# Optimization experiments

Measured on AMD Instinct MI355X. Metric: run time of the kernel, lower is better.

Reference implementation:

```python
import jax, jax.numpy as jnp
import numpy as np

N, E, IN_C, HID, HEADS, OUT_C, NG = 50000, 800000, 300, 64, 2, 2, 256


def _lin(key, fan_in, fan_out):
    k1, k2 = jax.random.split(key)
    lim = 1.0 / np.sqrt(fan_in)
    W = jax.random.uniform(k1, (fan_in, fan_out), jnp.float32, -lim, lim)
    b = jax.random.uniform(k2, (fan_out,), jnp.float32, -lim, lim)
    return W, b


def setup_inputs() -> dict:
    key = jax.random.key(0)
    ks = jax.random.split(key, 16)
    x = jax.random.normal(ks[0], (N, IN_C), jnp.float32)
    edge_index = jax.random.randint(ks[1], (2, E), 0, N, jnp.int64)
    batch = jnp.sort(jax.random.randint(ks[2], (N,), 0, NG, jnp.int64))
    d = {"x": x, "edge_index": edge_index, "batch": batch}
    d["syn_W"], d["syn_b"] = _lin(ks[3], IN_C, HID)
    d["ant_W"], d["ant_b"] = _lin(ks[4], IN_C, HID)
    d["fus_W"], d["fus_b"] = _lin(ks[5], 2 * HID, HID * HEADS)
    # conv1: in=HID*HEADS, out=HID, heads=HEADS (concat)
    d["c1_Wq"], d["c1_bq"] = _lin(ks[6], HID * HEADS, HEADS * HID)
    d["c1_Wk"], d["c1_bk"] = _lin(ks[7], HID * HEADS, HEADS * HID)
    d["c1_Wv"], d["c1_bv"] = _lin(ks[8], HID * HEADS, HEADS * HID)
    d["c1_Ws"], d["c1_bs"] = _lin(ks[9], HID * HEADS, HEADS * HID)
    # conv2: in=HID*HEADS, out=HID, heads=1
    d["c2_Wq"], d["c2_bq"] = _lin(ks[10], HID * HEADS, HID)
    d["c2_Wk"], d["c2_bk"] = _lin(ks[11], HID * HEADS, HID)
    d["c2_Wv"], d["c2_bv"] = _lin(ks[12], HID * HEADS, HID)
    d["c2_Ws"], d["c2_bs"] = _lin(ks[13], HID * HEADS, HID)
    d["l1_W"], d["l1_b"] = _lin(ks[14], HID, HID)
    d["l2_W"], d["l2_b"] = _lin(ks[15], HID, OUT_C)
    return d


def transformer_conv(x, src, dst, Wq, bq, Wk, bk, Wv, bv, Ws, bs, heads, d_head):
    # PyG TransformerConv (concat=True, root_weight=True, eval mode)
    q = (x @ Wq + bq).reshape(-1, heads, d_head)  # [N,H,D]
    k = (x @ Wk + bk).reshape(-1, heads, d_head)
    v = (x @ Wv + bv).reshape(-1, heads, d_head)
    qi = q[dst]  # [E,H,D]
    kj = k[src]
    vj = v[src]
    alpha = jnp.einsum("ehd,ehd->eh", qi, kj) / jnp.sqrt(jnp.float32(d_head))
    amax = jax.ops.segment_max(alpha, dst, num_segments=x.shape[0])
    ealpha = jnp.exp(alpha - amax[dst])
    denom = jax.ops.segment_sum(ealpha, dst, num_segments=x.shape[0])
    alpha = ealpha / (denom[dst] + 1e-16)
    out = jax.ops.segment_sum(alpha[..., None] * vj, dst, num_segments=x.shape[0])
    out = out.reshape(x.shape[0], heads * d_head)
    return out + x @ Ws + bs


def reference(x, edge_index, batch, syn_W, syn_b, ant_W, ant_b, fus_W, fus_b,
              c1_Wq, c1_bq, c1_Wk, c1_bk, c1_Wv, c1_bv, c1_Ws, c1_bs,
              c2_Wq, c2_bq, c2_Wk, c2_bk, c2_Wv, c2_bv, c2_Ws, c2_bs,
              l1_W, l1_b, l2_W, l2_b):
    src, dst = edge_index[0], edge_index[1]
    x_syn = jax.nn.relu(x @ syn_W + syn_b)
    x_ant = jax.nn.relu(x @ ant_W + ant_b)
    x_fused = jnp.concatenate([x_syn, x_ant], axis=1) @ fus_W + fus_b  # [N, HID*HEADS]
    h = transformer_conv(x_fused, src, dst, c1_Wq, c1_bq, c1_Wk, c1_bk,
                         c1_Wv, c1_bv, c1_Ws, c1_bs, HEADS, HID)
    h = jax.nn.relu(h)
    h = transformer_conv(h, src, dst, c2_Wq, c2_bq, c2_Wk, c2_bk,
                         c2_Wv, c2_bv, c2_Ws, c2_bs, 1, HID)
    # global mean pool over graphs
    sums = jax.ops.segment_sum(h, batch, num_segments=NG)
    cnts = jax.ops.segment_sum(jnp.ones((h.shape[0], 1), h.dtype), batch, num_segments=NG)
    pooled = sums / jnp.maximum(cnts, 1.0)
    out = jax.nn.relu(pooled @ l1_W + l1_b)
    return out @ l2_W + l2_b
```

## Files before the change

kernel.cpp:

```cpp
#include <hip/hip_runtime.h>
#include <math.h>

#define NNODES 50000
#define NEDGES 800000
#define INC    300
#define NGRAPH 256

typedef __attribute__((ext_vector_type(8))) short bf16x8;
typedef __attribute__((ext_vector_type(4))) short bf16x4;
typedef __attribute__((ext_vector_type(4))) float f32x4;

#define L2E8 0.180336880f
#define SW(row, k) ((k) ^ (((row) & 7) << 3))
#define EB 3125
#define FRONT_BLOCKS 782
#define FF_GRID (FRONT_BLOCKS + EB)

__device__ __forceinline__ unsigned short f2bf(float f) {
    unsigned u = __float_as_uint(f);
    u += 0x7fffu + ((u >> 16) & 1u);
    return (unsigned short)(u >> 16);
}
__device__ __forceinline__ float bf2f(unsigned short h) {
    return __uint_as_float(((unsigned)h) << 16);
}

struct WTArgs {
    const float* w[11];
    unsigned short* o[11];
    int K[11];
    int N[11];
    int mode[11];
    int roff[11];
    const float* syn_b; const float* ant_b;
    const float* c1q; const float* c1k; const float* c1v; const float* c1s;
    const float* c2q; const float* c2k; const float* c2v; const float* c2s;
    float* enc_b;
    float* c1_b;
    float* c2_b;
};

__global__ void k_setup(WTArgs a, const int* __restrict__ dstv, int* __restrict__ deg) {
    int bx = blockIdx.x;
    if (bx < EB) {
        int e = bx * 256 + threadIdx.x;
        if (e < NEDGES) atomicAdd(&deg[dstv[e]], 1);
        return;
    }
    bx -= EB;
    int which = bx / 75;
    int sub = bx - which * 75;
    if (which == 11) {
        if (sub != 0) return;
        int t = threadIdx.x;
        for (int u = t; u < 896; u += 256) {
            if (u < 512) {
                int s = u >> 7, r = u & 127;
                const float* p = (s == 0) ? a.c1q : (s == 1) ? a.c1k : (s == 2) ? a.c1v : a.c1s;
                a.c1_b[u] = p[r];
            } else if (u < 768) {
                int v = u - 512;
                int s = v >> 6, r = v & 63;
                const float* p = (s == 0) ? a.c2q : (s == 1) ? a.c2k : (s == 2) ? a.c2v : a.c2s;
                a.c2_b[v] = p[r];
            } else {
                int v = u - 768;
                a.enc_b[v] = (v < 64) ? a.syn_b[v] : a.ant_b[v - 64];
            }
        }
        return;
    }
    int i = sub * 256 + threadIdx.x;
    int K = a.K[which], N = a.N[which];
    if (i >= K * N) return;
    int k = i / N, n = i - k * N;
    unsigned short v = f2bf(a.w[which][i]);
    size_t dst;
    int m = a.mode[which];
    if (m == 1) {
        int row = a.roff[which] + n;
        dst = (size_t)(k >> 6) * 8192 + row * 64 + SW(row, k & 63);
    } else if (m == 2) {
        dst = (size_t)n * 128 + SW(n, k);
    } else {
        dst = (size_t)n * K + k;
    }
    a.o[which][dst] = v;
}

__global__ void k_scan1(const int* __restrict__ deg, int* __restrict__ ex,
                        int* __restrict__ bsum, int n) {
    __shared__ int tmp[256];
    int i = blockIdx.x * 256 + threadIdx.x;
    int v = (i < n) ? deg[i] : 0;
    tmp[threadIdx.x] = v;
    __syncthreads();
    for (int off = 1; off < 256; off <<= 1) {
        int t = (threadIdx.x >= off) ? tmp[threadIdx.x - off] : 0;
        __syncthreads();
        tmp[threadIdx.x] += t;
        __syncthreads();
    }
    if (i < n) ex[i] = tmp[threadIdx.x] - v;
    if (threadIdx.x == 255) bsum[blockIdx.x] = tmp[255];
}

__global__ void k_scan2(int* __restrict__ bsum, int nb) {
    __shared__ int tmp[256];
    int v = (threadIdx.x < nb) ? bsum[threadIdx.x] : 0;
    tmp[threadIdx.x] = v;
    __syncthreads();
    for (int off = 1; off < 256; off <<= 1) {
        int t = (threadIdx.x >= off) ? tmp[threadIdx.x - off] : 0;
        __syncthreads();
        tmp[threadIdx.x] += t;
        __syncthreads();
    }
    if (threadIdx.x < nb) bsum[threadIdx.x] = tmp[threadIdx.x] - v;
}

__global__ void k_scan3(int* __restrict__ rp, const int* __restrict__ bsum,
                        int* __restrict__ cursor, int n, int E) {
    int i = blockIdx.x * 256 + threadIdx.x;
    if (i < n) {
        int r = rp[i] + bsum[blockIdx.x];
        rp[i] = r;
        cursor[i] = r;
    }
    if (i == 0) rp[n] = E;
}

__global__ __launch_bounds__(256) void k_front_fill(
    const float* __restrict__ x,
    const unsigned short* __restrict__ enc_img, const float* __restrict__ enc_b,
    const unsigned short* __restrict__ fus_img, const float* __restrict__ fus_b,
    const unsigned short* __restrict__ c1_img, const float* __restrict__ c1_b,
    unsigned short* __restrict__ qkvs1, int M,
    const int* __restrict__ src, const int* __restrict__ dstv,
    int* __restrict__ cursor, int* __restrict__ esrc)
{
    const int b = blockIdx.x;
    const int q = b / 5, r5 = b - q * 5;
    const int tid = threadIdx.x;
    if (!(r5 == 0 && q < FRONT_BLOCKS)) {
        int nf = (b + 4) / 5;
        if (nf > FRONT_BLOCKS) nf = FRONT_BLOCKS;
        int e = (b - nf) * 256 + tid;
        if (e < NEDGES) {
            int d = dstv[e];
            int p = atomicAdd(&cursor[d], 1);
            esrc[p] = src[e];
        }
        return;
    }
    __shared__ __align__(16) short P[24576];
    short* bufI = P;
    short* B0   = P + 8192;
    short* B1   = P + 16384;
    short* Bt   = P + 8192;
    const int bm = q * 64;
    const int l  = tid & 63;
    const int wv = tid >> 6;
    const int fr = l & 15;
    const int fg = l >> 4;

    bf16x8 aP[10];
    {
        int row = bm + wv * 16 + fr;
        if (row >= M) row = M - 1;
        const float* xr = x + (size_t)row * INC + fg * 8;
        #pragma unroll
        for (int t = 0; t < 9; ++t) {
            float4 u0 = *reinterpret_cast<const float4*>(xr + t * 32);
            float4 u1 = *reinterpret_cast<const float4*>(xr + t * 32 + 4);
            bf16x8 f;
            f[0] = (short)f2bf(u0.x); f[1] = (short)f2bf(u0.y);
            f[2] = (short)f2bf(u0.z); f[3] = (short)f2bf(u0.w);
            f[4] = (short)f2bf(u1.x); f[5] = (short)f2bf(u1.y);
            f[6] = (short)f2bf(u1.z); f[7] = (short)f2bf(u1.w);
            aP[t] = f;
        }
        bf16x8 f9 = (bf16x8){0, 0, 0, 0, 0, 0, 0, 0};
        int c0 = 288 + fg * 8;
        #pragma unroll
        for (int j = 0; j < 8; ++j) {
            int c = c0 + j;
            if (c < INC) f9[j] = (short)f2bf(x[(size_t)row * INC + c]);
        }
        aP[9] = f9;
    }

    f32x4 acc1[8];
    #pragma unroll
    for (int j = 0; j < 8; ++j) acc1[j] = (f32x4){0.f, 0.f, 0.f, 0.f};

    {
        bf16x8* d = (bf16x8*)B0;
        const bf16x8* s = (const bf16x8*)enc_img;
        #pragma unroll
        for (int i = 0; i < 4; ++i) d[tid + i * 256] = s[tid + i * 256];
    }
    __syncthreads();
    for (int ph = 0; ph < 5; ++ph) {
        short* cur = (ph & 1) ? B1 : B0;
        short* nxt = (ph & 1) ? B0 : B1;
        bf16x8 tmp[4];
        if (ph < 4) {
            const bf16x8* s = (const bf16x8*)(enc_img + (ph + 1) * 8192);
            #pragma unroll
            for (int i = 0; i < 4; ++i) tmp[i] = s[tid + i * 256];
        }
        #pragma unroll
        for (int ks = 0; ks < 2; ++ks) {
            int kk = ks * 32 + fg * 8;
            int t = ph * 2 + ks;
            #pragma unroll
            for (int nj = 0; nj < 8; ++nj) {
                int br = nj * 16 + fr;
                bf16x8 bfr = *reinterpret_cast<const bf16x8*>(cur + br * 64 + SW(br, kk));
                acc1[nj] = __builtin_amdgcn_mfma_f32_16x16x32_bf16(aP[t], bfr, acc1[nj], 0, 0, 0);
            }
        }
        if (ph < 4) {
            bf16x8* d = (bf16x8*)nxt;
            #pragma unroll
            for (int i = 0; i < 4; ++i) d[tid + i * 256] = tmp[i];
        }
        __syncthreads();
    }
    #pragma unroll
    for (int nj = 0; nj < 8; ++nj) {
        int col = nj * 16 + fr;
        float bv = enc_b[col];
        #pragma unroll
        for (int r = 0; r < 4; ++r) {
            int row = wv * 16 + fg * 4 + r;
            float val = fmaxf(acc1[nj][r] + bv, 0.f);
            bufI[row * 128 + SW(row, col)] = (short)f2bf(val);
        }
    }
    __syncthreads();

    bf16x8 af[4];
    {
        int ar = wv * 16 + fr;
        #pragma unroll
        for (int t = 0; t < 4; ++t)
            af[t] = *reinterpret_cast<const bf16x8*>(bufI + ar * 128 + SW(ar, fg * 8 + t * 32));
    }
    __syncthreads();
    {
        bf16x8* d = (bf16x8*)Bt;
        const bf16x8* s = (const bf16x8*)fus_img;
        #pragma unroll
        for (int i = 0; i < 8; ++i) d[tid + i * 256] = s[tid + i * 256];
    }
    __syncthreads();

    f32x4 acc2[8];
    #pragma unroll
    for (int j = 0; j < 8; ++j) acc2[j] = (f32x4){0.f, 0.f, 0.f, 0.f};
    #pragma unroll
    for (int t = 0; t < 4; ++t) {
        int k = t * 32 + fg * 8;
        #pragma unroll
        for (int nj = 0; nj < 8; ++nj) {
            int br = nj * 16 + fr;
            bf16x8 bfr = *reinterpret_cast<const bf16x8*>(Bt + br * 128 + SW(br, k));
            acc2[nj] = __builtin_amdgcn_mfma_f32_16x16x32_bf16(af[t], bfr, acc2[nj], 0, 0, 0);
        }
    }
    __syncthreads();
    #pragma unroll
    for (int nj = 0; nj < 8; ++nj) {
        int col = nj * 16 + fr;
        float bv = fus_b[col];
        #pragma unroll
        for (int r = 0; r < 4; ++r) {
            int row = wv * 16 + fg * 4 + r;
            bufI[row * 128 + SW(row, col)] = (short)f2bf(acc2[nj][r] + bv);
        }
    }
    __syncthreads();

    bf16x8 af2[4];
    {
        int ar = wv * 16 + fr;
        #pragma unroll
        for (int t = 0; t < 4; ++t)
            af2[t] = *reinterpret_cast<const bf16x8*>(bufI + ar * 128 + SW(ar, fg * 8 + t * 32));
    }

    #pragma unroll
    for (int cc = 0; cc < 4; ++cc) {
        __syncthreads();
        {
            bf16x8* d = (bf16x8*)Bt;
            const bf16x8* s = (const bf16x8*)(c1_img + cc * 16384);
            #pragma unroll
            for (int i = 0; i < 8; ++i) d[tid + i * 256] = s[tid + i * 256];
        }
        __syncthreads();
        f32x4 acc3[8];
        #pragma unroll
        for (int j = 0; j < 8; ++j) acc3[j] = (f32x4){0.f, 0.f, 0.f, 0.f};
        #pragma unroll
        for (int t = 0; t < 4; ++t) {
            int k = t * 32 + fg * 8;
            #pragma unroll
            for (int nj = 0; nj < 8; ++nj) {
                int br = nj * 16 + fr;
                bf16x8 bfr = *reinterpret_cast<const bf16x8*>(Bt + br * 128 + SW(br, k));
                acc3[nj] = __builtin_amdgcn_mfma_f32_16x16x32_bf16(af2[t], bfr, acc3[nj], 0, 0, 0);
            }
        }
        #pragma unroll
        for (int nj = 0; nj < 8; ++nj) {
            int col = nj * 16 + fr;
            float bv = c1_b[cc * 128 + col];
            #pragma unroll
            for (int r = 0; r < 4; ++r) {
                int row = wv * 16 + fg * 4 + r;
                bufI[row * 128 + col] = (short)f2bf(acc3[nj][r] + bv);
            }
        }
        __syncthreads();
        #pragma unroll
        for (int i = 0; i < 4; ++i) {
            int p = tid + i * 256;
            int row = p >> 4;
            int c8 = (p & 15) * 8;
            int gr = bm + row;
            if (gr < M)
                *reinterpret_cast<bf16x8*>(qkvs1 + (size_t)gr * 512 + cc * 128 + c8) =
                    *reinterpret_cast<const bf16x8*>(bufI + row * 128 + c8);
        }
    }
}

#define BM 128

template<int BNT>
__global__ __launch_bounds__(256) void gemm_mfma(
    const unsigned short* __restrict__ A, int lda, int M, int K,
    const unsigned short* __restrict__ Wt,
    const float* __restrict__ bias,
    unsigned short* __restrict__ C, int ldc)
{
    __shared__ __align__(16) short As[BM * 64];
    __shared__ __align__(16) short Bs[BNT * 64];
    const int tid = threadIdx.x;
    const int bm = blockIdx.x * BM;
    const int bn = blockIdx.y * BNT;
    const int tr = tid >> 4;
    const int tc = (tid & 15) * 4;
    const int l  = tid & 63;
    const int wv = tid >> 6;
    const int fr = l & 15;
    const int fg = l >> 4;

    f32x4 acc[2][BNT / 16];
    #pragma unroll
    for (int i = 0; i < 2; ++i)
        #pragma unroll
        for (int j = 0; j < BNT / 16; ++j) acc[i][j] = (f32x4){0.f, 0.f, 0.f, 0.f};

    for (int k0 = 0; k0 < K; k0 += 64) {
        #pragma unroll
        for (int p = 0; p < 8; ++p) {
            int row = p * 16 + tr;
            int grow = bm + row;
            int k = k0 + tc;
            bf16x4 s4 = (bf16x4){0, 0, 0, 0};
            if (grow < M) s4 = *reinterpret_cast<const bf16x4*>(A + (size_t)grow * lda + k);
            *reinterpret_cast<bf16x4*>(As + row * 64 + SW(row, tc)) = s4;
        }
        #pragma unroll
        for (int p = 0; p < BNT / 16; ++p) {
            int n = p * 16 + tr;
            *reinterpret_cast<bf16x4*>(Bs + n * 64 + SW(n, tc)) =
                *reinterpret_cast<const bf16x4*>(Wt + (size_t)(bn + n) * K + k0 + tc);
        }
        __syncthreads();
        #pragma unroll
        for (int ks = 0; ks < 2; ++ks) {
            int kk = ks * 32 + fg * 8;
            int ar0 = wv * 32 + fr, ar1 = wv * 32 + 16 + fr;
            bf16x8 a0 = *reinterpret_cast<const bf16x8*>(As + ar0 * 64 + SW(ar0, kk));
            bf16x8 a1 = *reinterpret_cast<const bf16x8*>(As + ar1 * 64 + SW(ar1, kk));
            #pragma unroll
            for (int nj = 0; nj < BNT / 16; ++nj) {
                int br = nj * 16 + fr;
                bf16x8 b = *reinterpret_cast<const bf16x8*>(Bs + br * 64 + SW(br, kk));
                acc[0][nj] = __builtin_amdgcn_mfma_f32_16x16x32_bf16(a0, b, acc[0][nj], 0, 0, 0);
                acc[1][nj] = __builtin_amdgcn_mfma_f32_16x16x32_bf16(a1, b, acc[1][nj], 0, 0, 0);
            }
        }
        __syncthreads();
    }
    #pragma unroll
    for (int mi = 0; mi < 2; ++mi) {
        #pragma unroll
        for (int nj = 0; nj < BNT / 16; ++nj) {
            int col = nj * 16 + fr;
            float bv = bias[bn + col];
            #pragma unroll
            for (int r = 0; r < 4; ++r) {
                int lr = wv * 16 + fg * 4 + r;
                As[lr * BNT + col] = (short)f2bf(acc[mi][nj][r] + bv);
            }
        }
        __syncthreads();
        #pragma unroll
        for (int i = 0; i < 4; ++i) {
            int p = tid + i * 256;
            int lr = p >> 4;
            int c8 = (p & 15) * 8;
            int grow = bm + (lr >> 4) * 32 + mi * 16 + (lr & 15);
            if (grow < M)
                *reinterpret_cast<bf16x8*>(C + (size_t)grow * ldc + bn + c8) =
                    *reinterpret_cast<const bf16x8*>(As + lr * BNT + c8);
        }
        __syncthreads();
    }
}

__global__ __launch_bounds__(256) void attn_h2(
    const unsigned short* __restrict__ qkvs,
    const int* __restrict__ rowptr, const int* __restrict__ esrc,
    unsigned short* __restrict__ outp, int N)
{
    int wid = (blockIdx.x * blockDim.x + threadIdx.x) >> 6;
    int l = threadIdx.x & 63;
    if (wid >= N) return;
    const int sl = l & 15;
    const int g  = l >> 4;
    const unsigned short* bi = qkvs + (size_t)wid * 512;
    float q[8];
    {
        bf16x8 qv = *reinterpret_cast<const bf16x8*>(bi + 8 * sl);
        #pragma unroll
        for (int i = 0; i < 8; ++i) q[i] = bf2f((unsigned short)qv[i]) * L2E8;
    }
    float s = 0.f;
    float acc[8] = {0.f, 0.f, 0.f, 0.f, 0.f, 0.f, 0.f, 0.f};
    const int beg = rowptr[wid], end = rowptr[wid + 1];
    const int iters = (end - beg + 3) >> 2;
    int e = beg + g;
    bool va0 = e < end;
    int j0 = va0 ? esrc[e] : wid;
    const unsigned short* pp0 = qkvs + (size_t)j0 * 512 + 8 * sl;
    bf16x8 ka = *reinterpret_cast<const bf16x8*>(pp0 + 128);
    bf16x8 vva = *reinterpret_cast<const bf16x8*>(pp0 + 256);
    bool va1 = (e + 4) < end;
    int j1 = va1 ? esrc[e + 4] : wid;
    const unsigned short* pp1 = qkvs + (size_t)j1 * 512 + 8 * sl;
    bf16x8 kb = *reinterpret_cast<const bf16x8*>(pp1 + 128);
    bf16x8 vvb = *reinterpret_cast<const bf16x8*>(pp1 + 256);
    for (int it = 0; it < iters; ++it) {
        bf16x8 kc = ka, vc = vva;
        bool vd = va0;
        ka = kb; vva = vvb; va0 = va1;
        va1 = (e + 8) < end;
        int j2 = va1 ? esrc[e + 8] : wid;
        const unsigned short* p2 = qkvs + (size_t)j2 * 512 + 8 * sl;
        kb = *reinterpret_cast<const bf16x8*>(p2 + 128);
        vvb = *reinterpret_cast<const bf16x8*>(p2 + 256);
        e += 4;
        float p = 0.f;
        #pragma unroll
        for (int i = 0; i < 8; ++i) p += q[i] * bf2f((unsigned short)kc[i]);
        p += __shfl_xor(p, 1, 64);
        p += __shfl_xor(p, 2, 64);
        p += __shfl_xor(p, 4, 64);
        float w = vd ? __builtin_amdgcn_exp2f(p) : 0.f;
        s += w;
        #pragma unroll
        for (int i = 0; i < 8; ++i) acc[i] += w * bf2f((unsigned short)vc[i]);
    }
    #pragma unroll
    for (int mask = 16; mask <= 32; mask <<= 1) {
        s += __shfl_xor(s, mask, 64);
        #pragma unroll
        for (int i = 0; i < 8; ++i) acc[i] += __shfl_xor(acc[i], mask, 64);
    }
    if (g == 0) {
        float inv = 1.f / (s + 1e-16f);
        bf16x8 sv = *reinterpret_cast<const bf16x8*>(bi + 384 + 8 * sl);
        bf16x8 o;
        #pragma unroll
        for (int i = 0; i < 8; ++i) {
            float r = fmaxf(acc[i] * inv + bf2f((unsigned short)sv[i]), 0.f);
            o[i] = (short)f2bf(r);
        }
        *reinterpret_cast<bf16x8*>(outp + (size_t)wid * 128 + 8 * sl) = o;
    }
}

__global__ __launch_bounds__(256) void attn_h1(
    const unsigned short* __restrict__ qkvs,
    const int* __restrict__ rowptr, const int* __restrict__ esrc,
    float* __restrict__ outp, int N)
{
    int wid = (blockIdx.x * blockDim.x + threadIdx.x) >> 6;
    int l = threadIdx.x & 63;
    if (wid >= N) return;
    const int sl = l & 7;
    const int g  = l >> 3;
    const unsigned short* bi = qkvs + (size_t)wid * 256;
    float q[8];
    {
        bf16x8 qv = *reinterpret_cast<const bf16x8*>(bi + 8 * sl);
        #pragma unroll
        for (int i = 0; i < 8; ++i) q[i] = bf2f((unsigned short)qv[i]) * L2E8;
    }
    float s = 0.f;
    float acc[8] = {0.f, 0.f, 0.f, 0.f, 0.f, 0.f, 0.f, 0.f};
    const int beg = rowptr[wid], end = rowptr[wid + 1];
    const int iters = (end - beg + 7) >> 3;
    int e = beg + g;
    bool va0 = e < end;
    int j0 = va0 ? esrc[e] : wid;
    const unsigned short* pp0 = qkvs + (size_t)j0 * 256 + 8 * sl;
    bf16x8 ka = *reinterpret_cast<const bf16x8*>(pp0 + 64);
    bf16x8 vva = *reinterpret_cast<const bf16x8*>(pp0 + 128);
    bool va1 = (e + 8) < end;
    int j1 = va1 ? esrc[e + 8] : wid;
    const unsigned short* pp1 = qkvs + (size_t)j1 * 256 + 8 * sl;
    bf16x8 kb = *reinterpret_cast<const bf16x8*>(pp1 + 64);
    bf16x8 vvb = *reinterpret_cast<const bf16x8*>(pp1 + 128);
    for (int it = 0; it < iters; ++it) {
        bf16x8 kc = ka, vc = vva;
        bool vd = va0;
        ka = kb; vva = vvb; va0 = va1;
        va1 = (e + 16) < end;
        int j2 = va1 ? esrc[e + 16] : wid;
        const unsigned short* p2 = qkvs + (size_t)j2 * 256 + 8 * sl;
        kb = *reinterpret_cast<const bf16x8*>(p2 + 64);
        vvb = *reinterpret_cast<const bf16x8*>(p2 + 128);
        e += 8;
        float p = 0.f;
        #pragma unroll
        for (int i = 0; i < 8; ++i) p += q[i] * bf2f((unsigned short)kc[i]);
        p += __shfl_xor(p, 1, 64);
        p += __shfl_xor(p, 2, 64);
        p += __shfl_xor(p, 4, 64);
        float w = vd ? __builtin_amdgcn_exp2f(p) : 0.f;
        s += w;
        #pragma unroll
        for (int i = 0; i < 8; ++i) acc[i] += w * bf2f((unsigned short)vc[i]);
    }
    #pragma unroll
    for (int mask = 8; mask <= 32; mask <<= 1) {
        s += __shfl_xor(s, mask, 64);
        #pragma unroll
        for (int i = 0; i < 8; ++i) acc[i] += __shfl_xor(acc[i], mask, 64);
    }
    if (g == 0) {
        float inv = 1.f / (s + 1e-16f);
        float r[8];
        #pragma unroll
        for (int i = 0; i < 8; ++i)
            r[i] = acc[i] * inv + bf2f(bi[192 + 8 * sl + i]);
        float* op = outp + (size_t)wid * 64 + 8 * sl;
        *reinterpret_cast<float4*>(op)     = make_float4(r[0], r[1], r[2], r[3]);
        *reinterpret_cast<float4*>(op + 4) = make_float4(r[4], r[5], r[6], r[7]);
    }
}

__device__ __forceinline__ int lbound(const int* __restrict__ a, int n, int key) {
    int lo = 0, hi = n;
    while (lo < hi) {
        int mid = (lo + hi) >> 1;
        if (a[mid] < key) lo = mid + 1; else hi = mid;
    }
    return lo;
}

__global__ void pool_head(const float* __restrict__ h, const int* __restrict__ batch,
                          const float* __restrict__ l1W, const float* __restrict__ l1b,
                          const float* __restrict__ l2W, const float* __restrict__ l2b,
                          float* __restrict__ out) {
    __shared__ float red[4][64];
    int g = blockIdx.x;
    int l = threadIdx.x & 63;
    int w = threadIdx.x >> 6;
    int lo = lbound(batch, NNODES, g);
    int hi = lbound(batch, NNODES, g + 1);
    float s = 0.f;
    for (int i = lo + w; i < hi; i += 4) s += h[(size_t)i * 64 + l];
    red[w][l] = s;
    __syncthreads();
    if (w == 0) {
        float t = red[0][l] + red[1][l] + red[2][l] + red[3][l];
        float cnt = (float)((hi - lo) > 1 ? (hi - lo) : 1);
        float p = t / cnt;
        float hsum = l1b[l];
        #pragma unroll
        for (int kk = 0; kk < 64; ++kk) {
            float pk = __shfl(p, kk, 64);
            hsum += pk * l1W[kk * 64 + l];
        }
        float hr = fmaxf(hsum, 0.f);
        float o0 = hr * l2W[l * 2 + 0];
        float o1 = hr * l2W[l * 2 + 1];
        #pragma unroll
        for (int off = 32; off > 0; off >>= 1) {
            o0 += __shfl_xor(o0, off, 64);
            o1 += __shfl_xor(o1, off, 64);
        }
        if (l == 0) {
            out[g * 2 + 0] = o0 + l2b[0];
            out[g * 2 + 1] = o1 + l2b[1];
        }
    }
}

extern "C" void kernel_launch(void* const* d_in, const int* in_sizes, int n_in,
                              void* d_out, int out_size, void* d_ws, size_t ws_size,
                              hipStream_t stream) {
    const float* x      = (const float*)d_in[0];
    const int*   ei     = (const int*)d_in[1];
    const int*   batch  = (const int*)d_in[2];
    const float* syn_W  = (const float*)d_in[3];  const float* syn_b = (const float*)d_in[4];
    const float* ant_W  = (const float*)d_in[5];  const float* ant_b = (const float*)d_in[6];
    const float* fus_W  = (const float*)d_in[7];  const float* fus_b = (const float*)d_in[8];
    const float* c1_Wq  = (const float*)d_in[9];  const float* c1_bq = (const float*)d_in[10];
    const float* c1_Wk  = (const float*)d_in[11]; const float* c1_bk = (const float*)d_in[12];
    const float* c1_Wv  = (const float*)d_in[13]; const float* c1_bv = (const float*)d_in[14];
    const float* c1_Ws  = (const float*)d_in[15]; const float* c1_bs = (const float*)d_in[16];
    const float* c2_Wq  = (const float*)d_in[17]; const float* c2_bq = (const float*)d_in[18];
    const float* c2_Wk  = (const float*)d_in[19]; const float* c2_bk = (const float*)d_in[20];
    const float* c2_Wv  = (const float*)d_in[21]; const float* c2_bv = (const float*)d_in[22];
    const float* c2_Ws  = (const float*)d_in[23]; const float* c2_bs = (const float*)d_in[24];
    const float* l1_W   = (const float*)d_in[25]; const float* l1_b  = (const float*)d_in[26];
    const float* l2_W   = (const float*)d_in[27]; const float* l2_b  = (const float*)d_in[28];
    const int* src = ei;
    const int* dst = ei + NEDGES;
    float* out = (float*)d_out;

    char* ws = (char*)d_ws;
    size_t off = 0;
    auto alloc = [&](size_t bytes) -> char* {
        char* p = ws + off;
        off += (bytes + 255) & ~((size_t)255);
        return p;
    };

    unsigned short* H     = (unsigned short*)alloc((size_t)NNODES * 128 * 2);
    unsigned short* H2b   = (unsigned short*)alloc((size_t)NNODES * 128 * 2);
    unsigned short* qkvs1 = (unsigned short*)alloc((size_t)NNODES * 512 * 2);
    unsigned short* qkvs2 = (unsigned short*)alloc((size_t)NNODES * 256 * 2);
    unsigned short* enc_img = (unsigned short*)alloc((size_t)5 * 8192 * 2);
    unsigned short* fus_img = (unsigned short*)alloc((size_t)16384 * 2);
    unsigned short* c1_img  = (unsigned short*)alloc((size_t)4 * 16384 * 2);
    unsigned short* c2w_t   = (unsigned short*)alloc((size_t)256 * 128 * 2);
    float* enc_b = (float*)alloc(128 * 4);
    float* c1_b  = (float*)alloc(512 * 4);
    float* c2_b  = (float*)alloc(256 * 4);
    int*   deg    = (int*)alloc((NNODES + 1) * 4);
    int*   cursor = (int*)alloc((NNODES + 1) * 4);
    int*   rowptr = (int*)alloc((NNODES + 1) * 4);
    int*   bsum   = (int*)alloc(256 * 4);
    int*   esrc   = (int*)alloc((size_t)NEDGES * 4);

    const int NB = (NNODES + 255) / 256;
    dim3 t256(256);

    WTArgs wa;
    wa.w[0] = syn_W;  wa.o[0] = enc_img;  wa.K[0] = 300; wa.N[0] = 64;  wa.mode[0] = 1; wa.roff[0] = 0;
    wa.w[1] = ant_W;  wa.o[1] = enc_img;  wa.K[1] = 300; wa.N[1] = 64;  wa.mode[1] = 1; wa.roff[1] = 64;
    wa.w[2] = fus_W;  wa.o[2] = fus_img;  wa.K[2] = 128; wa.N[2] = 128; wa.mode[2] = 2; wa.roff[2] = 0;
    wa.w[3] = c1_Wq;  wa.o[3] = c1_img + 0 * 16384; wa.K[3] = 128; wa.N[3] = 128; wa.mode[3] = 2; wa.roff[3] = 0;
    wa.w[4] = c1_Wk;  wa.o[4] = c1_img + 1 * 16384; wa.K[4] = 128; wa.N[4] = 128; wa.mode[4] = 2; wa.roff[4] = 0;
    wa.w[5] = c1_Wv;  wa.o[5] = c1_img + 2 * 16384; wa.K[5] = 128; wa.N[5] = 128; wa.mode[5] = 2; wa.roff[5] = 0;
    wa.w[6] = c1_Ws;  wa.o[6] = c1_img + 3 * 16384; wa.K[6] = 128; wa.N[6] = 128; wa.mode[6] = 2; wa.roff[6] = 0;
    wa.w[7] = c2_Wq;  wa.o[7] = c2w_t + 0 * 64 * 128;  wa.K[7] = 128; wa.N[7] = 64; wa.mode[7] = 0; wa.roff[7] = 0;
    wa.w[8] = c2_Wk;  wa.o[8] = c2w_t + 1 * 64 * 128;  wa.K[8] = 128; wa.N[8] = 64; wa.mode[8] = 0; wa.roff[8] = 0;
    wa.w[9] = c2_Wv;  wa.o[9] = c2w_t + 2 * 64 * 128;  wa.K[9] = 128; wa.N[9] = 64; wa.mode[9] = 0; wa.roff[9] = 0;
    wa.w[10] = c2_Ws; wa.o[10] = c2w_t + 3 * 64 * 128; wa.K[10] = 128; wa.N[10] = 64; wa.mode[10] = 0; wa.roff[10] = 0;
    wa.syn_b = syn_b; wa.ant_b = ant_b;
    wa.c1q = c1_bq; wa.c1k = c1_bk; wa.c1v = c1_bv; wa.c1s = c1_bs;
    wa.c2q = c2_bq; wa.c2k = c2_bk; wa.c2v = c2_bv; wa.c2s = c2_bs;
    wa.enc_b = enc_b; wa.c1_b = c1_b; wa.c2_b = c2_b;

    hipMemsetAsync(deg, 0, (NNODES + 1) * sizeof(int), stream);
    hipMemsetAsync(enc_img, 0, (size_t)5 * 8192 * 2, stream);
    k_setup<<<EB + 900, t256, 0, stream>>>(wa, dst, deg);

    k_scan1<<<NB, t256, 0, stream>>>(deg, rowptr, bsum, NNODES);
    k_scan2<<<1, t256, 0, stream>>>(bsum, NB);
    k_scan3<<<NB, t256, 0, stream>>>(rowptr, bsum, cursor, NNODES, NEDGES);

    k_front_fill<<<FF_GRID, t256, 0, stream>>>(
        x, enc_img, enc_b, fus_img, fus_b, c1_img, c1_b, qkvs1, NNODES,
        src, dst, cursor, esrc);

    attn_h2<<<(NNODES * 64 + 255) / 256, t256, 0, stream>>>(qkvs1, rowptr, esrc, H, NNODES);

    gemm_mfma<128><<<dim3((NNODES + BM - 1) / BM, 2), t256, 0, stream>>>(
        H, 128, NNODES, 128, c2w_t, c2_b, qkvs2, 256);

    float* H2 = (float*)H2b;
    attn_h1<<<(NNODES * 64 + 255) / 256, t256, 0, stream>>>(qkvs2, rowptr, esrc, H2, NNODES);

    pool_head<<<NGRAPH, t256, 0, stream>>>(H2, batch, l1_W, l1_b, l2_W, l2_b, out);
}
```

Before: 253.0 us.

## Shrink front-end LDS footprint by staging weights in half-size chunks

The fused front-end encoder/fusion/conv1-projection kernel now uses a single 16 KB weight buffer instead of a 32 KB double buffer. The encoder weight panels are loaded one at a time with no prefetch, and the fusion and conv1 weight tiles are split into two 64-column halves loaded one after another. Cutting shared memory from 48 KB to 32 KB per block is meant to fit more blocks per CU. The cost is more barriers and the loss of global-load overlap in the encoder loop.

```diff
diff --git a/kernel.cpp b/kernel.cpp
--- a/kernel.cpp
+++ b/kernel.cpp
@@ -153,11 +153,9 @@
         }
         return;
     }
-    __shared__ __align__(16) short P[24576];
+    __shared__ __align__(16) short P[16384];
     short* bufI = P;
-    short* B0   = P + 8192;
-    short* B1   = P + 16384;
-    short* Bt   = P + 8192;
+    short* Bh   = P + 8192;
     const int bm = q * 64;
     const int l  = tid & 63;
     const int wv = tid >> 6;
@@ -194,22 +192,14 @@
     #pragma unroll
     for (int j = 0; j < 8; ++j) acc1[j] = (f32x4){0.f, 0.f, 0.f, 0.f};
 
-    {
-        bf16x8* d = (bf16x8*)B0;
-        const bf16x8* s = (const bf16x8*)enc_img;
-        #pragma unroll
-        for (int i = 0; i < 4; ++i) d[tid + i * 256] = s[tid + i * 256];
-    }
-    __syncthreads();
     for (int ph = 0; ph < 5; ++ph) {
-        short* cur = (ph & 1) ? B1 : B0;
-        short* nxt = (ph & 1) ? B0 : B1;
-        bf16x8 tmp[4];
-        if (ph < 4) {
-            const bf16x8* s = (const bf16x8*)(enc_img + (ph + 1) * 8192);
-            #pragma unroll
-            for (int i = 0; i < 4; ++i) tmp[i] = s[tid + i * 256];
-        }
+        {
+            bf16x8* d = (bf16x8*)Bh;
+            const bf16x8* s = (const bf16x8*)(enc_img + ph * 8192);
+            #pragma unroll
+            for (int i = 0; i < 4; ++i) d[tid + i * 256] = s[tid + i * 256];
+        }
+        __syncthreads();
         #pragma unroll
         for (int ks = 0; ks < 2; ++ks) {
             int kk = ks * 32 + fg * 8;
@@ -217,14 +207,9 @@
             #pragma unroll
             for (int nj = 0; nj < 8; ++nj) {
                 int br = nj * 16 + fr;
-                bf16x8 bfr = *reinterpret_cast<const bf16x8*>(cur + br * 64 + SW(br, kk));
+                bf16x8 bfr = *reinterpret_cast<const bf16x8*>(Bh + br * 64 + SW(br, kk));
                 acc1[nj] = __builtin_amdgcn_mfma_f32_16x16x32_bf16(aP[t], bfr, acc1[nj], 0, 0, 0);
             }
-        }
-        if (ph < 4) {
-            bf16x8* d = (bf16x8*)nxt;
-            #pragma unroll
-            for (int i = 0; i < 4; ++i) d[tid + i * 256] = tmp[i];
         }
         __syncthreads();
     }
@@ -248,39 +233,44 @@
         for (int t = 0; t < 4; ++t)
             af[t] = *reinterpret_cast<const bf16x8*>(bufI + ar * 128 + SW(ar, fg * 8 + t * 32));
     }
+
+    f32x4 acc2[8];
+    #pragma unroll
+    for (int j = 0; j < 8; ++j) acc2[j] = (f32x4){0.f, 0.f, 0.f, 0.f};
+    #pragma unroll
+    for (int h = 0; h < 2; ++h) {
+        __syncthreads();
+        {
+            bf16x8* d = (bf16x8*)Bh;
+            const bf16x8* s = (const bf16x8*)(fus_img + h * 64 * 128);
+            #pragma unroll
+            for (int i = 0; i < 4; ++i) d[tid + i * 256] = s[tid + i * 256];
+        }
+        __syncthreads();
+        #pragma unroll
+        for (int t = 0; t < 4; ++t) {
+            int k = t * 32 + fg * 8;
+            #pragma unroll
+            for (int nj = 0; nj < 4; ++nj) {
+                int br = nj * 16 + fr;
+                bf16x8 bfr = *reinterpret_cast<const bf16x8*>(Bh + br * 128 + SW(br, k));
+                acc2[h * 4 + nj] = __builtin_amdgcn_mfma_f32_16x16x32_bf16(af[t], bfr, acc2[h * 4 + nj], 0, 0, 0);
+            }
+        }
+    }
     __syncthreads();
-    {
-        bf16x8* d = (bf16x8*)Bt;
-        const bf16x8* s = (const bf16x8*)fus_img;
-        #pragma unroll
-        for (int i = 0; i < 8; ++i) d[tid + i * 256] = s[tid + i * 256];
-    }
-    __syncthreads();
-
-    f32x4 acc2[8];
-    #pragma unroll
-    for (int j = 0; j < 8; ++j) acc2[j] = (f32x4){0.f, 0.f, 0.f, 0.f};
-    #pragma unroll
-    for (int t = 0; t < 4; ++t) {
-        int k = t * 32 + fg * 8;
-        #pragma unroll
-        for (int nj = 0; nj < 8; ++nj) {
-            int br = nj * 16 + fr;
-            bf16x8 bfr = *reinterpret_cast<const bf16x8*>(Bt + br * 128 + SW(br, k));
-            acc2[nj] = __builtin_amdgcn_mfma_f32_16x16x32_bf16(af[t], bfr, acc2[nj], 0, 0, 0);
-        }
-    }
-    __syncthreads();
-    #pragma unroll
-    for (int nj = 0; nj < 8; ++nj) {
-        int col = nj * 16 + fr;
-        float bv = fus_b[col];
-        #pragma unroll
-        for (int r = 0; r < 4; ++r) {
-            int row = wv * 16 + fg * 4 + r;
-            bufI[row * 128 + SW(row, col)] = (short)f2bf(acc2[nj][r] + bv);
-        }
-    }
+    #pragma unroll
+    for (int h = 0; h < 2; ++h)
+        #pragma unroll
+        for (int nj = 0; nj < 4; ++nj) {
+            int col = h * 64 + nj * 16 + fr;
+            float bv = fus_b[col];
+            #pragma unroll
+            for (int r = 0; r < 4; ++r) {
+                int row = wv * 16 + fg * 4 + r;
+                bufI[row * 128 + SW(row, col)] = (short)f2bf(acc2[h * 4 + nj][r] + bv);
+            }
+        }
     __syncthreads();
 
     bf16x8 af2[4];
@@ -293,37 +283,42 @@
 
     #pragma unroll
     for (int cc = 0; cc < 4; ++cc) {
-        __syncthreads();
-        {
-            bf16x8* d = (bf16x8*)Bt;
-            const bf16x8* s = (const bf16x8*)(c1_img + cc * 16384);
-            #pragma unroll
-            for (int i = 0; i < 8; ++i) d[tid + i * 256] = s[tid + i * 256];
-        }
-        __syncthreads();
         f32x4 acc3[8];
         #pragma unroll
         for (int j = 0; j < 8; ++j) acc3[j] = (f32x4){0.f, 0.f, 0.f, 0.f};
         #pragma unroll
-        for (int t = 0; t < 4; ++t) {
-            int k = t * 32 + fg * 8;
-            #pragma unroll
-            for (int nj = 0; nj < 8; ++nj) {
-                int br = nj * 16 + fr;
-                bf16x8 bfr = *reinterpret_cast<const bf16x8*>(Bt + br * 128 + SW(br, k));
-                acc3[nj] = __builtin_amdgcn_mfma_f32_16x16x32_bf16(af2[t], bfr, acc3[nj], 0, 0, 0);
-            }
-        }
-        #pragma unroll
-        for (int nj = 0; nj < 8; ++nj) {
-            int col = nj * 16 + fr;
-            float bv = c1_b[cc * 128 + col];
-            #pragma unroll
-            for (int r = 0; r < 4; ++r) {
-                int row = wv * 16 + fg * 4 + r;
-                bufI[row * 128 + col] = (short)f2bf(acc3[nj][r] + bv);
-            }
-        }
+        for (int h = 0; h < 2; ++h) {
+            __syncthreads();
+            {
+                bf16x8* d = (bf16x8*)Bh;
+                const bf16x8* s = (const bf16x8*)(c1_img + cc * 16384 + h * 64 * 128);
+                #pragma unroll
+                for (int i = 0; i < 4; ++i) d[tid + i * 256] = s[tid + i * 256];
+            }
+            __syncthreads();
+            #pragma unroll
+            for (int t = 0; t < 4; ++t) {
+                int k = t * 32 + fg * 8;
+                #pragma unroll
+                for (int nj = 0; nj < 4; ++nj) {
+                    int br = nj * 16 + fr;
+                    bf16x8 bfr = *reinterpret_cast<const bf16x8*>(Bh + br * 128 + SW(br, k));
+                    acc3[h * 4 + nj] = __builtin_amdgcn_mfma_f32_16x16x32_bf16(af2[t], bfr, acc3[h * 4 + nj], 0, 0, 0);
+                }
+            }
+        }
+        #pragma unroll
+        for (int h = 0; h < 2; ++h)
+            #pragma unroll
+            for (int nj = 0; nj < 4; ++nj) {
+                int col = h * 64 + nj * 16 + fr;
+                float bv = c1_b[cc * 128 + col];
+                #pragma unroll
+                for (int r = 0; r < 4; ++r) {
+                    int row = wv * 16 + fg * 4 + r;
+                    bufI[row * 128 + col] = (short)f2bf(acc3[h * 4 + nj][r] + bv);
+                }
+            }
         __syncthreads();
         #pragma unroll
         for (int i = 0; i < 4; ++i) {
```

New measurement: 249.2 us. Within noise of the previous version (-1.5%).
